# Optimization experiments

Measured on AMD Instinct MI355X. Metric: run time of the kernel, lower is better.

The kernel has to match this reference:

```python
import jax, jax.numpy as jnp
import numpy as np
import math

EMSIZE = 1024
B, S = 4, 1024
N = B * S

def setup_inputs() -> dict:
    key = jax.random.key(0)
    k1, k2, k3, k4, k5 = jax.random.split(key, 5)
    x = jax.random.normal(k1, (B, S, EMSIZE), dtype=jnp.float32)
    mask = jax.random.randint(k2, (N, N), 0, 2, dtype=jnp.int32)
    # nn.Linear default init scale ~ 1/sqrt(fan_in); use small normal weights
    sc = 1.0 / math.sqrt(EMSIZE)
    Wq = jax.random.normal(k3, (EMSIZE, EMSIZE), dtype=jnp.float32) * sc
    Wk = jax.random.normal(k4, (EMSIZE, EMSIZE), dtype=jnp.float32) * sc
    Wv = jax.random.normal(k5, (EMSIZE, EMSIZE), dtype=jnp.float32) * sc
    return {"x": x, "mask": mask, "Wq": Wq, "Wk": Wk, "Wv": Wv}

def reference(x, mask, Wq, Wk, Wv):
    b, s, e = x.shape
    xf = x.reshape(b * s, e)                       # [N, E]
    q = xf @ Wq.T                                  # nn.Linear: x @ W^T
    k = xf @ Wk.T
    v = xf @ Wv.T
    sim = q @ k.T                                  # [N, N] full cross-batch scores
    sim = jnp.where(mask == 0, jnp.float32(-1e20), sim)
    # NOTE: original scales AFTER masking, matching masked_fill then divide
    attn = jax.nn.softmax(sim / math.sqrt(e), axis=-1)
    out = attn @ v                                 # [N, E]
    return out.reshape(b, s, e)
```

## Files before the change

### kernel.cpp

```cpp
#include <hip/hip_runtime.h>
#include <hip/hip_bf16.h>
#include <math.h>


typedef __attribute__((ext_vector_type(8))) __bf16 bf16x8;
typedef __attribute__((ext_vector_type(4))) __bf16 bf16x4;
typedef __attribute__((ext_vector_type(4))) float f32x4;

__device__ __forceinline__ void gload_lds16(const void* g, void* l) {
  __builtin_amdgcn_global_load_lds(
      (__attribute__((address_space(1))) void*)(g),
      (__attribute__((address_space(3))) void*)(l), 16, 0, 0);
}

#define WAITB(N) asm volatile("s_waitcnt vmcnt(" #N ")\ns_barrier" ::: "memory")

#define LDS_FRAG(base, r) \
  *(const bf16x8*)((base) + (r) * 32 + (((hi) ^ ((r) & 3)) * 8))

#define MM16(mq, AF)                                                        \
  __builtin_amdgcn_s_setprio(1);                                            \
  _Pragma("unroll") for (int m = 0; m < 4; ++m)                             \
    _Pragma("unroll") for (int n = 0; n < 4; ++n)                           \
      acc[(mq) * 4 + m][n] = __builtin_amdgcn_mfma_f32_16x16x32_bf16(       \
          AF[m], bfr[n], acc[(mq) * 4 + m][n], 0, 0, 0);                    \
  __builtin_amdgcn_s_setprio(0);

template <int MR, int NT>
__device__ __forceinline__ void g8_loop(const __bf16* __restrict__ A, long lda, long row0,
                                        const __bf16* __restrict__ B, long ldb, long col0,
                                        int kt0, __bf16* sA, __bf16* sB,
                                        f32x4 (&acc)[MR][4], int tid) {
  const int lane = tid & 63;
  const int w = tid >> 6;
  const int wr = w >> 2, wc = w & 3;
  const int lo = lane & 15, hi = lane >> 4;
  constexpr int ATILE = MR * 1024;
  constexpr int AL = MR / 4;

  auto stageA = [&](int buf, int kt) {
#pragma unroll
    for (int j = 0; j < AL; ++j) {
      int p = tid + j * 512;
      int row = p >> 2, cg = (p & 3) ^ (row & 3);
      gload_lds16(A + (row0 + row) * lda + kt * 32 + cg * 8,
                  sA + buf * ATILE + p * 8);
    }
  };
  auto stageB = [&](int buf, int kt) {
#pragma unroll
    for (int j = 0; j < 2; ++j) {
      int p = tid + j * 512;
      int row = p >> 2, cg = (p & 3) ^ (row & 3);
      gload_lds16(B + (col0 + row) * ldb + kt * 32 + cg * 8,
                  sB + buf * 8192 + p * 8);
    }
  };

#pragma unroll
  for (int t = 0; t < 3; ++t) { stageA(t, kt0 + t); stageB(t, kt0 + t); }
  if constexpr (MR == 8) { WAITB(8); } else { WAITB(6); }

  for (int t = 0; t < NT; ++t) {
    const int d = t & 3;
    const __bf16* sAc = sA + d * ATILE;
    const __bf16* sBc = sB + d * 8192;
    const int s = (t + 3) & 3;
    bf16x8 af[4], bfr[4];
#pragma unroll
    for (int m = 0; m < 4; ++m) af[m] = LDS_FRAG(sAc, wr * (MR * 16) + m * 16 + lo);
#pragma unroll
    for (int n = 0; n < 4; ++n) bfr[n] = LDS_FRAG(sBc, wc * 64 + n * 16 + lo);
    if (t + 3 < NT) stageA(s, kt0 + t + 3);
    if (MR == 4 && t + 3 < NT) stageB(s, kt0 + t + 3);
    __builtin_amdgcn_s_barrier();
    MM16(0, af);
    if constexpr (MR == 8) {
      __builtin_amdgcn_s_barrier();
      bf16x8 af2[4];
#pragma unroll
      for (int m = 0; m < 4; ++m) af2[m] = LDS_FRAG(sAc, wr * 128 + 64 + m * 16 + lo);
      if (t + 3 < NT) stageB(s, kt0 + t + 3);
      __builtin_amdgcn_s_barrier();
      MM16(1, af2);
    }
    if (t + 3 < NT)      { if constexpr (MR == 8) { WAITB(8); } else { WAITB(6); } }
    else if (t + 2 < NT) { if constexpr (MR == 8) { WAITB(4); } else { WAITB(3); } }
    else                 { WAITB(0); }
  }
}


__global__ __launch_bounds__(512) void qkv8(const __bf16* __restrict__ xb,
                                            const __bf16* __restrict__ wq,
                                            const __bf16* __restrict__ wk,
                                            const __bf16* __restrict__ wv,
                                            __bf16* __restrict__ qb,
                                            __bf16* __restrict__ kb,
                                            __bf16* __restrict__ vtb) {
  __shared__ __bf16 sA[4 * 8192];
  __shared__ __bf16 sB[4 * 8192];
  const int raw = blockIdx.x;
  const int wid = (raw & 7) * 24 + (raw >> 3);
  const int z = wid >> 6;
  const int r2 = wid & 63;
  const int tid = threadIdx.x;
  const __bf16* A;
  const __bf16* B;
  long row0, col0;
  if (z == 2) {
    A = wv; B = xb;
    row0 = (long)(r2 >> 4) * 256;
    col0 = (long)(r2 & 15) * 256;
  } else {
    A = xb; B = (z == 0) ? wq : wk;
    row0 = (long)(r2 >> 2) * 256;
    col0 = (long)(r2 & 3) * 256;
  }
  f32x4 acc[8][4] = {};
  g8_loop<8, 32>(A, 1024, row0, B, 1024, col0, 0, sA, sB, acc, tid);

  const int lane = tid & 63, w = tid >> 6;
  const int wr = w >> 2, wc = w & 3;
  const int lo = lane & 15, hi = lane >> 4;
#pragma unroll
  for (int m = 0; m < 8; ++m)
#pragma unroll
    for (int n = 0; n < 4; ++n)
#pragma unroll
      for (int i = 0; i < 4; ++i) {
        long r = row0 + wr * 128 + m * 16 + hi * 4 + i;
        long c = col0 + wc * 64 + n * 16 + lo;
        __bf16 v = (__bf16)acc[m][n][i];
        if (z == 0)      qb[r * 1024 + c] = v;
        else if (z == 1) kb[r * 1024 + c] = v;
        else             vtb[r * 4096 + c] = v;
      }
}

__global__ __launch_bounds__(512) void qk8(const __bf16* __restrict__ qb,
                                           const __bf16* __restrict__ kb,
                                           const int* __restrict__ mask,
                                           __bf16* __restrict__ attn,
                                           float* __restrict__ rowsum) {
  __shared__ __bf16 sA[4 * 8192];
  __shared__ __bf16 sB[4 * 8192];
  const int raw = blockIdx.x;
  const int wid = (raw & 7) * 32 + (raw >> 3);
  const long row0 = (long)(wid >> 4) * 256;
  const long col0 = (long)(wid & 15) * 256;
  const int tid = threadIdx.x;
  f32x4 acc[8][4] = {};
  g8_loop<8, 32>(qb, 1024, row0, kb, 1024, col0, 0, sA, sB, acc, tid);

  const int lane = tid & 63, w = tid >> 6;
  const int wr = w >> 2, wc = w & 3;
  const int lo = lane & 15, hi = lane >> 4;
#pragma unroll
  for (int m = 0; m < 8; ++m)
#pragma unroll
    for (int i = 0; i < 4; ++i) {
      long r = row0 + wr * 128 + m * 16 + hi * 4 + i;
      float s = 0.f;
#pragma unroll
      for (int n = 0; n < 4; ++n) {
        long c = col0 + wc * 64 + n * 16 + lo;
        int mk = mask[r * 4096 + c];
        float p = mk ? __expf(acc[m][n][i] * 0.03125f) : 0.f;
        attn[r * 4096 + c] = (__bf16)p;
        s += p;
      }
      s += __shfl_xor(s, 1); s += __shfl_xor(s, 2);
      s += __shfl_xor(s, 4); s += __shfl_xor(s, 8);
      if (lo == 0) atomicAdd(&rowsum[r], s);
    }
}

__global__ __launch_bounds__(512) void pv8(const __bf16* __restrict__ attn,
                                           const __bf16* __restrict__ vt,
                                           float* __restrict__ out,
                                           float* __restrict__ p1) {
  __shared__ __bf16 sA[4 * 4096];
  __shared__ __bf16 sB[4 * 8192];
  const int raw = blockIdx.x;
  const int wid = (raw & 7) * 32 + (raw >> 3);
  const int z = wid >> 7;
  const int r2 = wid & 127;
  const long row0 = (long)(r2 >> 2) * 128;
  const long col0 = (long)(r2 & 3) * 256;
  float* C = z ? p1 : out;
  const int tid = threadIdx.x;
  f32x4 acc[4][4] = {};
  g8_loop<4, 64>(attn, 4096, row0, vt, 4096, col0, z * 64, sA, sB, acc, tid);

  const int lane = tid & 63, w = tid >> 6;
  const int wr = w >> 2, wc = w & 3;
  const int lo = lane & 15, hi = lane >> 4;
#pragma unroll
  for (int m = 0; m < 4; ++m)
#pragma unroll
    for (int n = 0; n < 4; ++n)
#pragma unroll
      for (int i = 0; i < 4; ++i) {
        long r = row0 + wr * 64 + m * 16 + hi * 4 + i;
        long c = col0 + wc * 64 + n * 16 + lo;
        C[r * 1024 + c] = acc[m][n][i];
      }
}

__global__ __launch_bounds__(256) void reduce_add2(float* __restrict__ out,
                                                   const float* __restrict__ p1,
                                                   const float* __restrict__ rs) {
  int i = blockIdx.x * 256 + threadIdx.x;
  int row = i >> 8;
  float inv = 1.0f / rs[row];
  float4 a = ((const float4*)out)[i];
  float4 b = ((const float4*)p1)[i];
  a.x = (a.x + b.x) * inv; a.y = (a.y + b.y) * inv;
  a.z = (a.z + b.z) * inv; a.w = (a.w + b.w) * inv;
  ((float4*)out)[i] = a;
}

__global__ __launch_bounds__(256) void cvt_all(const float* __restrict__ x,
                                               const float* __restrict__ wq,
                                               const float* __restrict__ wk,
                                               const float* __restrict__ wv,
                                               __bf16* __restrict__ xb,
                                               __bf16* __restrict__ wqb,
                                               __bf16* __restrict__ wkb,
                                               __bf16* __restrict__ wvb,
                                               float* __restrict__ rowsum) {
  int b = blockIdx.x;
  if (b >= 7168) {
#pragma unroll
    for (int j = 0; j < 16; ++j) rowsum[threadIdx.x * 16 + j] = 0.f;
    return;
  }
  const float* in;
  __bf16* out;
  int base;
  if (b < 4096)      { in = x;  out = xb;  base = b; }
  else if (b < 5120) { in = wq; out = wqb; base = b - 4096; }
  else if (b < 6144) { in = wk; out = wkb; base = b - 5120; }
  else               { in = wv; out = wvb; base = b - 6144; }
  int i = base * 256 + threadIdx.x;
  float4 f = ((const float4*)in)[i];
  bf16x4 o;
  o[0] = (__bf16)f.x; o[1] = (__bf16)f.y; o[2] = (__bf16)f.z; o[3] = (__bf16)f.w;
  ((bf16x4*)out)[i] = o;
}

extern "C" void kernel_launch(void* const* d_in, const int* in_sizes, int n_in,
                              void* d_out, int out_size, void* d_ws, size_t ws_size,
                              hipStream_t stream) {
  const float* x = (const float*)d_in[0];
  const int* mask = (const int*)d_in[1];
  const float* Wq = (const float*)d_in[2];
  const float* Wk = (const float*)d_in[3];
  const float* Wv = (const float*)d_in[4];
  float* out = (float*)d_out;

  char* ws = (char*)d_ws;
  __bf16* vtb = (__bf16*)(ws);
  __bf16* xb  = (__bf16*)(ws + (8ull << 20));
  __bf16* wqb = (__bf16*)(ws + (16ull << 20));
  __bf16* wkb = (__bf16*)(ws + (18ull << 20));
  __bf16* wvb = (__bf16*)(ws + (20ull << 20));
  __bf16* qb  = (__bf16*)(ws + (22ull << 20));
  __bf16* kb  = (__bf16*)(ws + (30ull << 20));
  __bf16* attn = (__bf16*)(ws + (38ull << 20));
  float*  rowsum = (float*)(ws + (70ull << 20));
  float*  p1  = (float*)(ws + (8ull << 20));

  cvt_all<<<7169, 256, 0, stream>>>(x, Wq, Wk, Wv, xb, wqb, wkb, wvb, rowsum);

  dim3 blk(512);
  qkv8<<<192, blk, 0, stream>>>(xb, wqb, wkb, wvb, qb, kb, vtb);
  qk8<<<256, blk, 0, stream>>>(qb, kb, mask, attn, rowsum);
  pv8<<<256, blk, 0, stream>>>(attn, vtb, out, p1);
  reduce_add2<<<4096, 256, 0, stream>>>(out, p1, rowsum);
}
```

Before: 157.7 us.

## Stage QK scores through LDS for vectorized mask/attn I/O; change LDS swizzle

The QK kernel epilogue now writes the accumulator tile to shared memory as bf16, then each thread reads a contiguous half-row and processes it with 128-bit mask loads and 128-bit bf16 attn stores. This replaces scattered 4-byte mask loads and 2-byte stores, and it cuts the rowsum atomics from one per 16-lane group per row fragment to one per row. The LDS swizzle also changes from row&3 to (row>>1)&3 to reduce bank conflicts on fragment reads. In exchange, the scores are rounded to bf16 before the exp, which loses some precision, and the epilogue gains an extra LDS round trip and a barrier.

New measurement: 157.7 us. No clear change (-0.0%).

```diff
diff --git a/kernel.cpp b/kernel.cpp
--- a/kernel.cpp
+++ b/kernel.cpp
@@ -16,7 +16,7 @@
 #define WAITB(N) asm volatile("s_waitcnt vmcnt(" #N ")\ns_barrier" ::: "memory")
 
 #define LDS_FRAG(base, r) \
-  *(const bf16x8*)((base) + (r) * 32 + (((hi) ^ ((r) & 3)) * 8))
+  *(const bf16x8*)((base) + (r) * 32 + (((hi) ^ (((r) >> 1) & 3)) * 8))
 
 #define MM16(mq, AF)                                                        \
   __builtin_amdgcn_s_setprio(1);                                            \
@@ -42,7 +42,7 @@
 #pragma unroll
     for (int j = 0; j < AL; ++j) {
       int p = tid + j * 512;
-      int row = p >> 2, cg = (p & 3) ^ (row & 3);
+      int row = p >> 2, cg = (p & 3) ^ ((row >> 1) & 3);
       gload_lds16(A + (row0 + row) * lda + kt * 32 + cg * 8,
                   sA + buf * ATILE + p * 8);
     }
@@ -51,7 +51,7 @@
 #pragma unroll
     for (int j = 0; j < 2; ++j) {
       int p = tid + j * 512;
-      int row = p >> 2, cg = (p & 3) ^ (row & 3);
+      int row = p >> 2, cg = (p & 3) ^ ((row >> 1) & 3);
       gload_lds16(B + (col0 + row) * ldb + kt * 32 + cg * 8,
                   sB + buf * 8192 + p * 8);
     }
@@ -143,15 +143,14 @@
                                            const int* __restrict__ mask,
                                            __bf16* __restrict__ attn,
                                            float* __restrict__ rowsum) {
-  __shared__ __bf16 sA[4 * 8192];
-  __shared__ __bf16 sB[4 * 8192];
+  __shared__ __bf16 smem[65536];
   const int raw = blockIdx.x;
   const int wid = (raw & 7) * 32 + (raw >> 3);
   const long row0 = (long)(wid >> 4) * 256;
   const long col0 = (long)(wid & 15) * 256;
   const int tid = threadIdx.x;
   f32x4 acc[8][4] = {};
-  g8_loop<8, 32>(qb, 1024, row0, kb, 1024, col0, 0, sA, sB, acc, tid);
+  g8_loop<8, 32>(qb, 1024, row0, kb, 1024, col0, 0, smem, smem + 32768, acc, tid);
 
   const int lane = tid & 63, w = tid >> 6;
   const int wr = w >> 2, wc = w & 3;
@@ -159,21 +158,39 @@
 #pragma unroll
   for (int m = 0; m < 8; ++m)
 #pragma unroll
-    for (int i = 0; i < 4; ++i) {
-      long r = row0 + wr * 128 + m * 16 + hi * 4 + i;
-      float s = 0.f;
-#pragma unroll
-      for (int n = 0; n < 4; ++n) {
-        long c = col0 + wc * 64 + n * 16 + lo;
-        int mk = mask[r * 4096 + c];
-        float p = mk ? __expf(acc[m][n][i] * 0.03125f) : 0.f;
-        attn[r * 4096 + c] = (__bf16)p;
-        s += p;
-      }
-      s += __shfl_xor(s, 1); s += __shfl_xor(s, 2);
-      s += __shfl_xor(s, 4); s += __shfl_xor(s, 8);
-      if (lo == 0) atomicAdd(&rowsum[r], s);
-    }
+    for (int n = 0; n < 4; ++n)
+#pragma unroll
+      for (int i = 0; i < 4; ++i)
+        smem[(wr * 128 + m * 16 + hi * 4 + i) * 256 + wc * 64 + n * 16 + lo] =
+            (__bf16)acc[m][n][i];
+  __syncthreads();
+  const int rr = tid >> 1, hh = tid & 1;
+  const long gr = row0 + rr;
+  const long gc = col0 + hh * 128;
+  const __bf16* srow = smem + rr * 256 + hh * 128;
+  const int4* mrow = (const int4*)(mask + gr * 4096 + gc);
+  __bf16* arow = attn + gr * 4096 + gc;
+  float s = 0.f;
+#pragma unroll
+  for (int j = 0; j < 16; ++j) {
+    bf16x8 v = ((const bf16x8*)srow)[j];
+    int4 m0 = mrow[2 * j], m1 = mrow[2 * j + 1];
+    float p[8];
+    p[0] = m0.x ? __expf((float)v[0] * 0.03125f) : 0.f;
+    p[1] = m0.y ? __expf((float)v[1] * 0.03125f) : 0.f;
+    p[2] = m0.z ? __expf((float)v[2] * 0.03125f) : 0.f;
+    p[3] = m0.w ? __expf((float)v[3] * 0.03125f) : 0.f;
+    p[4] = m1.x ? __expf((float)v[4] * 0.03125f) : 0.f;
+    p[5] = m1.y ? __expf((float)v[5] * 0.03125f) : 0.f;
+    p[6] = m1.z ? __expf((float)v[6] * 0.03125f) : 0.f;
+    p[7] = m1.w ? __expf((float)v[7] * 0.03125f) : 0.f;
+    bf16x8 o;
+#pragma unroll
+    for (int e = 0; e < 8; ++e) { o[e] = (__bf16)p[e]; s += p[e]; }
+    ((bf16x8*)arow)[j] = o;
+  }
+  s += __shfl_xor(s, 1);
+  if (hh == 0) atomicAdd(&rowsum[gr], s);
 }
 
 __global__ __launch_bounds__(512) void pv8(const __bf16* __restrict__ attn,
```
